# Kernel tuning notes

Measured on AMD Instinct MI355X. Metric: run time of the kernel, lower is better.

## Reference

```python
import jax, jax.numpy as jnp
import numpy as np
from jax import lax

UNIT = 0.11  # pairing threshold from sort_w(weight, 0.11)


def _greedy_pairs(wflat, unit=UNIT):
    """Faithful greedy pairing from sort_w: for each out-channel dd, scan flat
    indices a ascending; pair a with the first unoccupied b>a with
    |w[a]+w[b]|<=unit. Returns gather indices src and signs such that
    Weff[dd,i] = sign[dd,i] * Wflat[dd, src[dd,i]] reproduces vicsum_v2."""
    d, m = wflat.shape
    src = np.tile(np.arange(m, dtype=np.int32), (d, 1))
    sign = np.ones((d, m), dtype=np.float32)
    for dd in range(d):
        occ = np.zeros(m, dtype=bool)
        row = wflat[dd]
        for a in range(m - 1):
            if occ[a]:
                continue
            cand = np.nonzero((~occ[a + 1:]) & (np.abs(row[a] + row[a + 1:]) <= unit))[0]
            if cand.size:
                b = a + 1 + int(cand[0])
                occ[a] = occ[b] = True
                src[dd, b] = a     # out += (x[a]-x[b])*w[a]  =>  coeff at b is -w[a]
                sign[dd, b] = -1.0
    return src, sign


def _make_conv(rng, d, c, k):
    bound = 1.0 / np.sqrt(c * k * k)  # torch default uniform init scale
    w = rng.uniform(-bound, bound, size=(d, c, k, k)).astype(np.float32)
    b = rng.uniform(-bound, bound, size=(d,)).astype(np.float32)
    src, sign = _greedy_pairs(w.reshape(d, -1))
    return w, b, src, sign


def setup_inputs() -> dict:
    rng = np.random.default_rng(0)
    x = rng.standard_normal((16384, 1, 32, 32)).astype(np.float32)
    w1, b1, src1, sign1 = _make_conv(rng, 6, 1, 5)
    w2, b2, src2, sign2 = _make_conv(rng, 16, 6, 5)
    w3, b3, src3, sign3 = _make_conv(rng, 120, 16, 5)
    bf1 = 1.0 / np.sqrt(120.0)
    fc1_w = rng.uniform(-bf1, bf1, size=(84, 120)).astype(np.float32)
    fc1_b = rng.uniform(-bf1, bf1, size=(84,)).astype(np.float32)
    bf2 = 1.0 / np.sqrt(84.0)
    fc2_w = rng.uniform(-bf2, bf2, size=(10, 84)).astype(np.float32)
    fc2_b = rng.uniform(-bf2, bf2, size=(10,)).astype(np.float32)
    return {
        'x': jnp.asarray(x),
        'w1': jnp.asarray(w1), 'b1': jnp.asarray(b1), 'sign1': jnp.asarray(sign1),
        'w2': jnp.asarray(w2), 'b2': jnp.asarray(b2), 'sign2': jnp.asarray(sign2),
        'w3': jnp.asarray(w3), 'b3': jnp.asarray(b3), 'sign3': jnp.asarray(sign3),
        'fc1_w': jnp.asarray(fc1_w), 'fc1_b': jnp.asarray(fc1_b),
        'fc2_w': jnp.asarray(fc2_w), 'fc2_b': jnp.asarray(fc2_b),
        'src1': jnp.asarray(src1), 'src2': jnp.asarray(src2), 'src3': jnp.asarray(src3),
        'TRIGGERed': 1, 'count': 0,
    }


def _eff_weight(w, src, sign):
    d = w.shape[0]
    wflat = w.reshape(d, -1)
    weff = jnp.take_along_axis(wflat, src, axis=1) * sign
    return weff.reshape(w.shape)


def _conv(x, w, b):
    y = lax.conv_general_dilated(x, w, window_strides=(1, 1), padding='VALID',
                                 dimension_numbers=('NCHW', 'OIHW', 'NCHW'))
    return y + b[None, :, None, None]


def _avgpool2(x):
    n, c, h, w = x.shape
    return x.reshape(n, c, h // 2, 2, w // 2, 2).mean(axis=(3, 5))


def reference(x, w1, b1, sign1, w2, b2, sign2, w3, b3, sign3,
              fc1_w, fc1_b, fc2_w, fc2_b, src1, src2, src3, TRIGGERed, count):
    if TRIGGERed:
        h = _avgpool2(jax.nn.sigmoid(_conv(x, _eff_weight(w1, src1, sign1), b1)))
        h = _avgpool2(jax.nn.sigmoid(_conv(h, _eff_weight(w2, src2, sign2), b2)))
        h = jax.nn.sigmoid(_conv(h, _eff_weight(w3, src3, sign3), b3))
    else:
        h = _avgpool2(jax.nn.sigmoid(_conv(x, w1, b1)))
        h = _avgpool2(jax.nn.sigmoid(_conv(h, w2, b2)))
        h = jax.nn.sigmoid(_conv(h, w3, b3))
    h = h.reshape(h.shape[0], -1)                     # [N, 120]
    h = jax.nn.sigmoid(h @ fc1_w.T + fc1_b)           # [N, 84]
    return h @ fc2_w.T + fc2_b                        # [N, 10]
```

## Files before the change

kernel.cpp:

```cpp
#include <hip/hip_runtime.h>

#define THREADS 256

__device__ __forceinline__ float sigmoidf(float x) {
    return __builtin_amdgcn_rcpf(1.0f + __expf(-x));
}

#define E2OFF 168
#define E3OFF 2856
#define P1OFF 54056

__global__ void weff_prep(const float* __restrict__ w1, const float* __restrict__ sg1, const int* __restrict__ sr1,
                          const float* __restrict__ w2, const float* __restrict__ sg2, const int* __restrict__ sr2,
                          const float* __restrict__ w3, const float* __restrict__ sg3, const int* __restrict__ sr3,
                          const int* __restrict__ trig, float* __restrict__ ws) {
    int i = blockIdx.x * blockDim.x + threadIdx.x;
    const int t = trig[0];
    if (i < 168) {
        int c = i / 28, k = i % 28;
        float v = 0.f;
        if (k < 25) { int f = c * 25 + k; v = t ? sg1[f] * w1[c * 25 + sr1[f]] : w1[f]; }
        ws[i] = v;
    } else if (i < E3OFF) {
        int j = i - E2OFF;
        int oc = j / 168, r = j % 168, ic = r / 28, k = r % 28;
        float v = 0.f;
        if (k < 25) { int f = oc * 150 + ic * 25 + k; v = t ? sg2[f] * w2[oc * 150 + sr2[f]] : w2[f]; }
        ws[i] = v;
    } else if (i < P1OFF) {
        int idx = i - E3OFF;
        if (idx < 48000) {
            int q  = idx & 3;
            int j  = (idx >> 2) & 1;
            int tt = (idx >> 3) % 120;
            int k  = idx / 960;
            int c  = 2 * (tt >> 1) + j;
            int h  = tt & 1;
            int e  = c * 400 + h * 200 + 4 * k + q;
            ws[i] = t ? sg3[e] * w3[c * 400 + sr3[e]] : w3[e];
        } else {
            ws[i] = 0.f;
        }
    }
}

__global__ __launch_bounds__(THREADS, 4)
void k_conv1(const float* __restrict__ x, const float* __restrict__ ws,
             const float* __restrict__ b1, float* __restrict__ p1, int nimg) {
    __shared__ __align__(16) float lw[176];
    const int tid = threadIdx.x;
    if (tid < 168) lw[tid] = ws[tid];
    if (tid >= 168 && tid < 174) lw[tid] = b1[tid - 168];
    __syncthreads();

    int g = blockIdx.x * THREADS + tid;
    if (g >= nimg * 98) return;
    const int img = g / 98, rem = g % 98;
    const int r = rem / 7, t = rem % 7;

    const float* xb = x + (size_t)img * 1024 + (2 * r) * 32 + 4 * t;
    float pt[6][8];
    #pragma unroll
    for (int rr = 0; rr < 6; ++rr) {
        const float4 v0 = *reinterpret_cast<const float4*>(xb + rr * 32);
        const float4 v1 = *reinterpret_cast<const float4*>(xb + rr * 32 + 4);
        pt[rr][0] = v0.x; pt[rr][1] = v0.y; pt[rr][2] = v0.z; pt[rr][3] = v0.w;
        pt[rr][4] = v1.x; pt[rr][5] = v1.y; pt[rr][6] = v1.z; pt[rr][7] = v1.w;
    }

    #pragma unroll
    for (int c = 0; c < 6; ++c) {
        float z[2][4];
        #pragma unroll
        for (int p = 0; p < 2; ++p)
            #pragma unroll
            for (int w = 0; w < 4; ++w) z[p][w] = 0.f;

        #pragma unroll
        for (int k4 = 0; k4 < 6; ++k4) {
            const float4 w4 = *reinterpret_cast<const float4*>(&lw[c * 28 + 4 * k4]);
            #pragma unroll
            for (int j = 0; j < 4; ++j) {
                const int k = 4 * k4 + j;
                const int ky = k / 5, kx = k % 5;
                const float wv = (j == 0) ? w4.x : (j == 1) ? w4.y : (j == 2) ? w4.z : w4.w;
                #pragma unroll
                for (int p = 0; p < 2; ++p)
                    #pragma unroll
                    for (int dy = 0; dy < 2; ++dy)
                        #pragma unroll
                        for (int dx = 0; dx < 2; ++dx)
                            z[p][2 * dy + dx] += pt[dy + ky][2 * p + dx + kx] * wv;
            }
        }
        {
            const float wv = lw[c * 28 + 24];
            #pragma unroll
            for (int p = 0; p < 2; ++p)
                #pragma unroll
                for (int dy = 0; dy < 2; ++dy)
                    #pragma unroll
                    for (int dx = 0; dx < 2; ++dx)
                        z[p][2 * dy + dx] += pt[dy + 4][2 * p + dx + 4] * wv;
        }

        const float bb = lw[168 + c];
        const float s0 = sigmoidf(z[0][0] + bb) + sigmoidf(z[0][1] + bb) +
                         sigmoidf(z[0][2] + bb) + sigmoidf(z[0][3] + bb);
        const float s1 = sigmoidf(z[1][0] + bb) + sigmoidf(z[1][1] + bb) +
                         sigmoidf(z[1][2] + bb) + sigmoidf(z[1][3] + bb);
        *reinterpret_cast<float2*>(&p1[((size_t)img * 6 + c) * 196 + r * 14 + 2 * t]) =
            make_float2(0.25f * s0, 0.25f * s1);
    }
}

__global__ __launch_bounds__(THREADS, 3)
void k_conv2(const float* __restrict__ p1, const float* __restrict__ ws,
             const float* __restrict__ b2, float* __restrict__ p2, int nimg) {
    int g = blockIdx.x * THREADS + threadIdx.x;
    if (g >= nimg * 50) return;
    const int img = g / 50, rem = g % 50;
    const int pix = rem >> 1, di = rem & 1;
    const int pi = pix / 5, pj = pix % 5;
    const float* pimg = p1 + (size_t)img * 1176 + (2 * pi + di) * 14 + 2 * pj;
    const float* wq = ws + E2OFF;

    float acc[16][2];
    #pragma unroll
    for (int oc = 0; oc < 16; ++oc) { acc[oc][0] = 0.f; acc[oc][1] = 0.f; }

    #pragma unroll 2
    for (int ic = 0; ic < 6; ++ic) {
        float pt[5][6];
        const float* pb = pimg + ic * 196;
        #pragma unroll
        for (int r = 0; r < 5; ++r) {
            #pragma unroll
            for (int cc = 0; cc < 3; ++cc) {
                float2 v = *reinterpret_cast<const float2*>(pb + r * 14 + 2 * cc);
                pt[r][2 * cc] = v.x; pt[r][2 * cc + 1] = v.y;
            }
        }
        #pragma unroll
        for (int oc = 0; oc < 16; ++oc) {
            const float* wr = wq + oc * 168 + ic * 28;
            #pragma unroll
            for (int k4 = 0; k4 < 6; ++k4) {
                const float4 w4 = *reinterpret_cast<const float4*>(wr + 4 * k4);
                #pragma unroll
                for (int j = 0; j < 4; ++j) {
                    const int k = 4 * k4 + j;
                    const int ky = k / 5, kx = k % 5;
                    const float wv = (j == 0) ? w4.x : (j == 1) ? w4.y : (j == 2) ? w4.z : w4.w;
                    acc[oc][0] += pt[ky][kx] * wv;
                    acc[oc][1] += pt[ky][kx + 1] * wv;
                }
            }
            const float wv = wr[24];
            acc[oc][0] += pt[4][4] * wv;
            acc[oc][1] += pt[4][5] * wv;
        }
    }

    #pragma unroll
    for (int oc = 0; oc < 16; ++oc) {
        const float bb = b2[oc];
        float s = sigmoidf(acc[oc][0] + bb) + sigmoidf(acc[oc][1] + bb);
        s += __shfl_xor(s, 1, 64);
        if (di == 0)
            p2[(size_t)img * 400 + oc * 25 + pix] = 0.25f * s;
    }
}

#define T_IMG 8
__global__ __launch_bounds__(128, 4)
void k_tail(const float* __restrict__ p2, const float* __restrict__ ws,
            const float* __restrict__ b3,
            const float* __restrict__ fc1w, const float* __restrict__ fc1b,
            const float* __restrict__ fc2w, const float* __restrict__ fc2b,
            float* __restrict__ out, int nimg) {
    __shared__ __align__(16) float sp2[T_IMG][400];
    __shared__ __align__(16) float v3[T_IMG][120];
    __shared__ __align__(16) float v4[T_IMG][84];
    const int tid = threadIdx.x;
    const int img0 = blockIdx.x * T_IMG;

    for (int i = tid; i < T_IMG * 100; i += 128) {
        const int im = i / 100, off = i % 100;
        const int gi = min(img0 + im, nimg - 1);
        reinterpret_cast<float4*>(&sp2[im][0])[off] =
            reinterpret_cast<const float4*>(p2 + (size_t)gi * 400)[off];
    }
    __syncthreads();

    if (tid < 120) {
        const int h = tid & 1;
        const int cpair = tid >> 1;
        float acc[2][T_IMG];
        #pragma unroll
        for (int j = 0; j < 2; ++j)
            #pragma unroll
            for (int im = 0; im < T_IMG; ++im) acc[j][im] = 0.f;

        const float4* wp = reinterpret_cast<const float4*>(ws + E3OFF);
        #pragma unroll 2
        for (int k = 0; k < 50; ++k) {
            const float4 w0 = wp[(k * 120 + tid) * 2];
            const float4 w1 = wp[(k * 120 + tid) * 2 + 1];
            #pragma unroll
            for (int im = 0; im < T_IMG; ++im) {
                const float4 u = *reinterpret_cast<const float4*>(&sp2[im][h * 200 + 4 * k]);
                acc[0][im] += w0.x * u.x + w0.y * u.y + w0.z * u.z + w0.w * u.w;
                acc[1][im] += w1.x * u.x + w1.y * u.y + w1.z * u.z + w1.w * u.w;
            }
        }
        #pragma unroll
        for (int j = 0; j < 2; ++j) {
            const int c = 2 * cpair + j;
            const float bb = b3[c];
            #pragma unroll
            for (int im = 0; im < T_IMG; ++im) {
                float s = acc[j][im];
                s += __shfl_xor(s, 1, 64);
                if (h == 0) v3[im][c] = sigmoidf(s + bb);
            }
        }
    }
    __syncthreads();

    for (int it = tid; it < T_IMG * 84; it += 128) {
        const int im = it / 84, j = it % 84;
        const float4* wp = reinterpret_cast<const float4*>(fc1w + j * 120);
        const float4* vp = reinterpret_cast<const float4*>(&v3[im][0]);
        float4 a = make_float4(0.f, 0.f, 0.f, 0.f);
        #pragma unroll 6
        for (int k = 0; k < 30; ++k) {
            const float4 w4 = wp[k];
            const float4 u = vp[k];
            a.x += u.x * w4.x; a.y += u.y * w4.y;
            a.z += u.z * w4.z; a.w += u.w * w4.w;
        }
        v4[im][j] = sigmoidf((a.x + a.y) + (a.z + a.w) + fc1b[j]);
    }
    __syncthreads();

    if (tid < T_IMG * 10) {
        const int im = tid / 10, j = tid % 10;
        if (img0 + im < nimg) {
            const float4* wp = reinterpret_cast<const float4*>(fc2w + j * 84);
            const float4* vp = reinterpret_cast<const float4*>(&v4[im][0]);
            float4 a = make_float4(0.f, 0.f, 0.f, 0.f);
            #pragma unroll
            for (int k = 0; k < 21; ++k) {
                const float4 w4 = wp[k];
                const float4 u = vp[k];
                a.x += u.x * w4.x; a.y += u.y * w4.y;
                a.z += u.z * w4.z; a.w += u.w * w4.w;
            }
            out[(size_t)(img0 + im) * 10 + j] = (a.x + a.y) + (a.z + a.w) + fc2b[j];
        }
    }
}

__device__ __forceinline__ float wget_ig(const float* __restrict__ wp,
                                         const float* __restrict__ sg,
                                         const int* __restrict__ sr,
                                         int row, int m, int idx, bool tg) {
    int f = row * m + idx;
    return tg ? sg[f] * wp[row * m + sr[f]] : wp[f];
}

__global__ __launch_bounds__(THREADS, 4)
void lenet_fused(const float* __restrict__ x,
                 const float* __restrict__ w1e, const float* __restrict__ b1,
                 const float* __restrict__ w2e, const float* __restrict__ b2,
                 const float* __restrict__ w3e, const float* __restrict__ b3,
                 const float* __restrict__ fc1w, const float* __restrict__ fc1b,
                 const float* __restrict__ fc2w, const float* __restrict__ fc2b,
                 const float* __restrict__ sg1, const int* __restrict__ sr1,
                 const float* __restrict__ sg2, const int* __restrict__ sr2,
                 const float* __restrict__ sg3, const int* __restrict__ sr3,
                 const int* __restrict__ trig,
                 float* __restrict__ out, int nimg) {
    const int tid = threadIdx.x;
    const int img0 = blockIdx.x * 2;
    __shared__ __align__(16) float xs[2][1024];
    __shared__ __align__(16) float p1[2][6][196];
    __shared__ __align__(16) float p2[2][400];
    __shared__ __align__(16) float v3[2][120];
    __shared__ __align__(16) float v4[2][84];
    const bool tg = trig[0] != 0;

    #pragma unroll
    for (int im = 0; im < 2; ++im) {
        int gi = min(img0 + im, nimg - 1);
        reinterpret_cast<float4*>(&xs[im][0])[tid] =
            reinterpret_cast<const float4*>(x + (size_t)gi * 1024)[tid];
    }
    __syncthreads();

    for (int it = tid; it < 2 * 196; it += THREADS) {
        const int img = it / 196, pix = it % 196;
        const int pi = pix / 14, pj = pix % 14;
        const float* xb = &xs[img][(2 * pi) * 32 + 2 * pj];
        float pt[6][6];
        #pragma unroll
        for (int r = 0; r < 6; ++r)
            #pragma unroll
            for (int cc = 0; cc < 3; ++cc) {
                float2 v = *reinterpret_cast<const float2*>(&xb[r * 32 + cc * 2]);
                pt[r][cc * 2] = v.x; pt[r][cc * 2 + 1] = v.y;
            }
        #pragma unroll
        for (int c = 0; c < 6; ++c) {
            float z0 = 0.f, z1 = 0.f, z2 = 0.f, z3 = 0.f;
            #pragma unroll
            for (int ky = 0; ky < 5; ++ky)
                #pragma unroll
                for (int kx = 0; kx < 5; ++kx) {
                    const float wv = wget_ig(w1e, sg1, sr1, c, 25, ky * 5 + kx, tg);
                    z0 += pt[ky][kx] * wv;     z1 += pt[ky][kx + 1] * wv;
                    z2 += pt[ky + 1][kx] * wv; z3 += pt[ky + 1][kx + 1] * wv;
                }
            const float bb = b1[c];
            p1[img][c][pix] = 0.25f * (sigmoidf(z0 + bb) + sigmoidf(z1 + bb) +
                                       sigmoidf(z2 + bb) + sigmoidf(z3 + bb));
        }
    }
    __syncthreads();

    if (tid < 200) {
        const int img = tid / 100, rem = tid % 100;
        const int pix = rem >> 2, win = rem & 3;
        const int di = win >> 1, dj = win & 1;
        const int pi = pix / 5, pj = pix % 5;
        const int r0 = 2 * pi + di, c0 = 2 * pj + dj;
        float acc[16];
        #pragma unroll
        for (int c = 0; c < 16; ++c) acc[c] = 0.f;
        for (int ic = 0; ic < 6; ++ic) {
            float pt[5][5];
            #pragma unroll
            for (int ky = 0; ky < 5; ++ky)
                #pragma unroll
                for (int kx = 0; kx < 5; ++kx)
                    pt[ky][kx] = p1[img][ic][(r0 + ky) * 14 + (c0 + kx)];
            #pragma unroll
            for (int c = 0; c < 16; ++c) {
                float z = acc[c];
                #pragma unroll
                for (int ky = 0; ky < 5; ++ky)
                    #pragma unroll
                    for (int kx = 0; kx < 5; ++kx)
                        z += pt[ky][kx] * wget_ig(w2e, sg2, sr2, c, 150, ic * 25 + ky * 5 + kx, tg);
                acc[c] = z;
            }
        }
        #pragma unroll
        for (int c = 0; c < 16; ++c) {
            float z = sigmoidf(acc[c] + b2[c]);
            z += __shfl_xor(z, 1, 64);
            z += __shfl_xor(z, 2, 64);
            if (win == 0) p2[img][c * 25 + pix] = 0.25f * z;
        }
    }
    __syncthreads();

    if (tid < 240) {
        const int c = tid >> 1, h = tid & 1;
        float s0 = 0.f, s1 = 0.f;
        for (int k = 0; k < 200; ++k) {
            float wv = wget_ig(w3e, sg3, sr3, c, 400, h * 200 + k, tg);
            s0 += p2[0][h * 200 + k] * wv;
            s1 += p2[1][h * 200 + k] * wv;
        }
        s0 += __shfl_xor(s0, 1, 64);
        s1 += __shfl_xor(s1, 1, 64);
        if (h == 0) {
            const float bb = b3[c];
            v3[0][c] = sigmoidf(s0 + bb);
            v3[1][c] = sigmoidf(s1 + bb);
        }
    }
    __syncthreads();

    if (tid < 168) {
        const int img = tid / 84, j = tid % 84;
        float a = 0.f;
        for (int k = 0; k < 120; ++k) a += v3[img][k] * fc1w[j * 120 + k];
        v4[img][j] = sigmoidf(a + fc1b[j]);
    }
    __syncthreads();

    if (tid < 20) {
        const int img = tid / 10, j = tid % 10;
        if (img0 + img < nimg) {
            float a = 0.f;
            for (int k = 0; k < 84; ++k) a += v4[img][k] * fc2w[j * 84 + k];
            out[(size_t)(img0 + img) * 10 + j] = a + fc2b[j];
        }
    }
}

extern "C" void kernel_launch(void* const* d_in, const int* in_sizes, int n_in,
                              void* d_out, int out_size, void* d_ws, size_t ws_size,
                              hipStream_t stream) {
    const float* x    = (const float*)d_in[0];
    const float* w1   = (const float*)d_in[1];
    const float* b1   = (const float*)d_in[2];
    const float* sg1  = (const float*)d_in[3];
    const float* w2   = (const float*)d_in[4];
    const float* b2   = (const float*)d_in[5];
    const float* sg2  = (const float*)d_in[6];
    const float* w3   = (const float*)d_in[7];
    const float* b3   = (const float*)d_in[8];
    const float* sg3  = (const float*)d_in[9];
    const float* fc1w = (const float*)d_in[10];
    const float* fc1b = (const float*)d_in[11];
    const float* fc2w = (const float*)d_in[12];
    const float* fc2b = (const float*)d_in[13];
    const int*   sr1  = (const int*)d_in[14];
    const int*   sr2  = (const int*)d_in[15];
    const int*   sr3  = (const int*)d_in[16];
    const int*   trig = (const int*)d_in[17];

    const int nimg = in_sizes[0] / 1024;
    float* out = (float*)d_out;

    const size_t p1off = P1OFF;
    const size_t p2off = p1off + (size_t)nimg * 1176;
    const size_t need_bytes = (p2off + (size_t)nimg * 400) * sizeof(float);

    if (ws_size >= need_bytes) {
        float* ws = (float*)d_ws;
        weff_prep<<<(P1OFF + 255) / 256, 256, 0, stream>>>(
            w1, sg1, sr1, w2, sg2, sr2, w3, sg3, sr3, trig, ws);
        k_conv1<<<(nimg * 98 + THREADS - 1) / THREADS, THREADS, 0, stream>>>(
            x, ws, b1, ws + p1off, nimg);
        k_conv2<<<(nimg * 50 + THREADS - 1) / THREADS, THREADS, 0, stream>>>(
            ws + p1off, ws, b2, ws + p2off, nimg);
        k_tail<<<(nimg + T_IMG - 1) / T_IMG, 128, 0, stream>>>(
            ws + p2off, ws, b3, fc1w, fc1b, fc2w, fc2b, out, nimg);
    } else {
        lenet_fused<<<(nimg + 1) / 2, THREADS, 0, stream>>>(
            x, w1, b1, w2, b2, w3, b3,
            fc1w, fc1b, fc2w, fc2b, sg1, sr1, sg2, sr2, sg3, sr3, trig, out, nimg);
    }
}
```

Measured before the change: 228.8 us.

## Use packed fp16 dot2 for conv2 rows 0-3 with repacked weight layout

Conv2 now converts input rows 0-3 into packed half2 pairs and accumulates them with v_dot2 fp16 instructions into fp32 accumulators. Row 4 stays in fp32. The weight prep kernel repacks conv2 weights into a 16-slot per (oc,ic) layout holding fp16 pairs plus fp32 row-4 values. This roughly halves the FMA instruction count in the dominant conv2 loop, but fp16 rounding (round-toward-zero for inputs) lowers accuracy and the ic loop is no longer unrolled.

```diff
diff --git a/kernel.cpp b/kernel.cpp
--- a/kernel.cpp
+++ b/kernel.cpp
@@ -1,9 +1,20 @@
 #include <hip/hip_runtime.h>
 
 #define THREADS 256
+
+typedef _Float16 half2v __attribute__((ext_vector_type(2)));
+typedef __fp16   half2p __attribute__((ext_vector_type(2)));
 
 __device__ __forceinline__ float sigmoidf(float x) {
     return __builtin_amdgcn_rcpf(1.0f + __expf(-x));
+}
+
+__device__ __forceinline__ half2v f2h2(float f) {
+    union { float f; half2v h; } u; u.f = f; return u.h;
+}
+
+__device__ __forceinline__ half2v pk2h2(half2p p) {
+    union { half2p p; half2v h; } u; u.p = p; return u.h;
 }
 
 #define E2OFF 168
@@ -21,12 +32,29 @@
         float v = 0.f;
         if (k < 25) { int f = c * 25 + k; v = t ? sg1[f] * w1[c * 25 + sr1[f]] : w1[f]; }
         ws[i] = v;
+    } else if (i < 1704) {
+        int j = i - E2OFF;
+        int oc = j / 96, r = j % 96, ic = r / 16, slot = r % 16;
+        const int base = oc * 150 + ic * 25;
+        float outv = 0.f;
+        if (slot < 10) {
+            int kx = slot >> 1, p = slot & 1;
+            int k0 = base + (2 * p) * 5 + kx;
+            int k1 = base + (2 * p + 1) * 5 + kx;
+            float v0 = t ? sg2[k0] * w2[oc * 150 + sr2[k0]] : w2[k0];
+            float v1 = t ? sg2[k1] * w2[oc * 150 + sr2[k1]] : w2[k1];
+            union { _Float16 h[2]; float f; } pun;
+            pun.h[0] = (_Float16)v0;
+            pun.h[1] = (_Float16)v1;
+            outv = pun.f;
+        } else if (slot < 15) {
+            int kx = slot - 10;
+            int k4 = base + 20 + kx;
+            outv = t ? sg2[k4] * w2[oc * 150 + sr2[k4]] : w2[k4];
+        }
+        ws[i] = outv;
     } else if (i < E3OFF) {
-        int j = i - E2OFF;
-        int oc = j / 168, r = j % 168, ic = r / 28, k = r % 28;
-        float v = 0.f;
-        if (k < 25) { int f = oc * 150 + ic * 25 + k; v = t ? sg2[f] * w2[oc * 150 + sr2[f]] : w2[f]; }
-        ws[i] = v;
+        ws[i] = 0.f;
     } else if (i < P1OFF) {
         int idx = i - E3OFF;
         if (idx < 48000) {
@@ -129,7 +157,6 @@
     #pragma unroll
     for (int oc = 0; oc < 16; ++oc) { acc[oc][0] = 0.f; acc[oc][1] = 0.f; }
 
-    #pragma unroll 2
     for (int ic = 0; ic < 6; ++ic) {
         float pt[5][6];
         const float* pb = pimg + ic * 196;
@@ -141,24 +168,27 @@
                 pt[r][2 * cc] = v.x; pt[r][2 * cc + 1] = v.y;
             }
         }
+        half2v pk01[6], pk23[6];
+        #pragma unroll
+        for (int cc = 0; cc < 6; ++cc) {
+            pk01[cc] = pk2h2(__builtin_amdgcn_cvt_pkrtz(pt[0][cc], pt[1][cc]));
+            pk23[cc] = pk2h2(__builtin_amdgcn_cvt_pkrtz(pt[2][cc], pt[3][cc]));
+        }
         #pragma unroll
         for (int oc = 0; oc < 16; ++oc) {
-            const float* wr = wq + oc * 168 + ic * 28;
-            #pragma unroll
-            for (int k4 = 0; k4 < 6; ++k4) {
-                const float4 w4 = *reinterpret_cast<const float4*>(wr + 4 * k4);
-                #pragma unroll
-                for (int j = 0; j < 4; ++j) {
-                    const int k = 4 * k4 + j;
-                    const int ky = k / 5, kx = k % 5;
-                    const float wv = (j == 0) ? w4.x : (j == 1) ? w4.y : (j == 2) ? w4.z : w4.w;
-                    acc[oc][0] += pt[ky][kx] * wv;
-                    acc[oc][1] += pt[ky][kx + 1] * wv;
-                }
-            }
-            const float wv = wr[24];
-            acc[oc][0] += pt[4][4] * wv;
-            acc[oc][1] += pt[4][5] * wv;
+            const float* wrow = wq + (oc * 6 + ic) * 16;
+            #pragma unroll
+            for (int kx = 0; kx < 5; ++kx) {
+                const half2v wa = f2h2(wrow[2 * kx]);
+                const half2v wb = f2h2(wrow[2 * kx + 1]);
+                const float  wf = wrow[10 + kx];
+                acc[oc][0] = __builtin_amdgcn_fdot2(pk01[kx], wa, acc[oc][0], false);
+                acc[oc][0] = __builtin_amdgcn_fdot2(pk23[kx], wb, acc[oc][0], false);
+                acc[oc][0] += pt[4][kx] * wf;
+                acc[oc][1] = __builtin_amdgcn_fdot2(pk01[kx + 1], wa, acc[oc][1], false);
+                acc[oc][1] = __builtin_amdgcn_fdot2(pk23[kx + 1], wb, acc[oc][1], false);
+                acc[oc][1] += pt[4][kx + 1] * wf;
+            }
         }
     }
 
```

New measurement: 220.0 us, median of 2. 3.8% less time.
